# Kernel optimization log

Hardware: AMD Instinct MI355X
Metric: run time of the kernel (lower is better)

The kernel has to match this reference:

```python
import jax, jax.numpy as jnp
import numpy as np
from jax import lax

DN = ('NCHW', 'OIHW', 'NCHW')
BN_EPS = 1e-5
LRELU_SLOPE = 0.01


def conv_block(x, w1, b1, w2, b2, gamma, bn_bias):
    # Conv2d(512->256, k=1) -> Conv2d(256->512, k=3, pad=1) -> LeakyReLU -> BatchNorm2d(512)
    y = lax.conv_general_dilated(x, w1, (1, 1), 'VALID', dimension_numbers=DN)
    y = y + b1[None, :, None, None]
    y = lax.conv_general_dilated(y, w2, (1, 1), 'SAME', dimension_numbers=DN)
    y = y + b2[None, :, None, None]
    y = jnp.where(y > 0, y, LRELU_SLOPE * y)
    # BatchNorm2d in training mode: batch statistics over (B, H, W) per channel
    mean = jnp.mean(y, axis=(0, 2, 3))
    var = jnp.var(y, axis=(0, 2, 3))
    y = (y - mean[None, :, None, None]) * lax.rsqrt(var + BN_EPS)[None, :, None, None]
    return y * gamma[None, :, None, None] + bn_bias[None, :, None, None]


def setup_inputs() -> dict:
    key = jax.random.key(0)
    ks = jax.random.split(key, 9)
    B, C, H, W = 8, 512, 32, 32
    x = jax.random.normal(ks[0], (B, C, H, W), dtype=jnp.float32)
    x1 = jax.random.normal(ks[1], (B, C, H, W), dtype=jnp.float32)
    x2 = jax.random.normal(ks[2], (B, C, H, W), dtype=jnp.float32)
    w1 = jax.random.normal(ks[3], (256, 512, 1, 1), dtype=jnp.float32) * 0.02
    b1 = jnp.zeros((256,), dtype=jnp.float32)
    w2 = jax.random.normal(ks[4], (512, 256, 3, 3), dtype=jnp.float32) * 0.02
    b2 = jnp.zeros((512,), dtype=jnp.float32)
    gamma = jnp.ones((512,), dtype=jnp.float32)
    bn_bias = jnp.zeros((512,), dtype=jnp.float32)
    beta = jax.random.normal(ks[5], (1,), dtype=jnp.float32)  # Parameter(zeros(1)) in torch; random so output is non-trivial
    return {"x": x, "x1": x1, "x2": x2, "w1": w1, "b1": b1, "w2": w2,
            "b2": b2, "gamma": gamma, "bn_bias": bn_bias, "beta": beta}


def reference(x, x1, x2, w1, b1, w2, b2, gamma, bn_bias, beta):
    B, C, H, W = x1.shape
    N = H * W
    F1 = conv_block(x1, w1, b1, w2, b2, gamma, bn_bias).reshape(B, C, N)   # [B, C, N]
    F2 = conv_block(x2, w1, b1, w2, b2, gamma, bn_bias).reshape(B, C, N)   # [B, C, N]
    scores = jnp.einsum('bcn,bdn->bcd', F1, F2)                            # [B, C, C]
    attention = jax.nn.softmax(scores, axis=-1)
    out = jnp.einsum('bcd,bdn->bcn', attention, x.reshape(B, C, N))
    return beta * out.reshape(B, C, H, W)
```

## Files before the change

### kernel.cpp

```cpp
#include <hip/hip_runtime.h>


typedef __attribute__((ext_vector_type(8))) short bfrag;
typedef __attribute__((ext_vector_type(4))) float facc;

__device__ __forceinline__ unsigned short bf16_rn(float v) {
  unsigned u = __float_as_uint(v);
  return (unsigned short)((u + 0x7fffu + ((u >> 16) & 1u)) >> 16);
}

__device__ __forceinline__ void dma16(const void* g, const void* lds) {
  __builtin_amdgcn_global_load_lds(
      (const __attribute__((address_space(1))) unsigned int*)g,
      (__attribute__((address_space(3))) unsigned int*)(unsigned int)(unsigned long long)(const char*)lds,
      16, 0, 0);
}

__global__ __launch_bounds__(256) void prologue(
    const float* __restrict__ x1, const float* __restrict__ x2,
    const float* __restrict__ w2, unsigned char* __restrict__ x12timg,
    unsigned short* __restrict__ w2s, float* __restrict__ statsz) {
  int bid = blockIdx.x;
  int t = threadIdx.x;
  if (bid < 8192) {
    __shared__ float tile[32][33];
    int p0 = (bid & 31) * 32, ci0 = ((bid >> 5) & 15) * 32, z = bid >> 9;
    const float* src = (z < 8) ? x1 + (size_t)z * 524288 : x2 + (size_t)(z - 8) * 524288;
    {
      int ci_l = t >> 5, p_l = t & 31;
#pragma unroll
      for (int j = 0; j < 4; j++)
        tile[ci_l + 8 * j][p_l] = src[(size_t)(ci0 + ci_l + 8 * j) * 1024 + p0 + p_l];
    }
    __syncthreads();
    {
      int p_l = t >> 3, cg = (t & 7) * 4;
      unsigned short hh[4], ll[4];
#pragma unroll
      for (int j = 0; j < 4; j++) {
        float v = tile[cg + j][p_l];
        hh[j] = bf16_rn(v);
        ll[j] = bf16_rn(v - __uint_as_float((unsigned)hh[j] << 16));
      }
      int px = p0 + p_l, row = px & 127, panel = px >> 7;
      int c = ci0 + cg, kc = c >> 6, ck = (c >> 3) & 7;
      int slot = ck ^ (row & 7);
      size_t byte = (((size_t)(z * 8 + panel) * 8 + kc) * 128 + row) * 256 + slot * 16 + (c & 7) * 2;
      *(ushort4*)(x12timg + byte) = make_ushort4(hh[0], hh[1], hh[2], hh[3]);
      *(ushort4*)(x12timg + byte + 128) = make_ushort4(ll[0], ll[1], ll[2], ll[3]);
    }
  } else {
    int co = bid - 8192;
    if (co < 40) statsz[co * 256 + t] = 0.f;
    int panel = co >> 7, co_l = co & 127;
    int chunk = t >> 5, q = (t >> 3) & 3, e = t & 7;
    int slot = q ^ (co_l & 7);
    const float* src = w2 + ((size_t)co * 256 + t) * 9;
#pragma unroll
    for (int tap = 0; tap < 9; tap++) {
      float v = src[tap];
      unsigned short h = bf16_rn(v);
      unsigned short l = bf16_rn(v - __uint_as_float((unsigned)h << 16));
      int P = (panel * 8 + chunk) * 9 + tap;
      size_t us = (size_t)P * 8192 + co_l * 64 + slot * 8 + e;
      w2s[us] = h;
      w2s[us ^ 32] = l;
    }
  }
}

__global__ __launch_bounds__(256) void transpose_split_x(
    const float* __restrict__ x, unsigned char* __restrict__ img) {
  __shared__ float tile[32][33];
  int z = blockIdx.z;
  const float* src = x + (size_t)z * 524288;
  int ci0 = blockIdx.y * 32, p0 = blockIdx.x * 32;
  int t = threadIdx.x;
  {
    int ci_l = t >> 5, p_l = t & 31;
#pragma unroll
    for (int j = 0; j < 4; j++)
      tile[ci_l + 8 * j][p_l] = src[(size_t)(ci0 + ci_l + 8 * j) * 1024 + p0 + p_l];
  }
  __syncthreads();
  {
    int p_l = t >> 3, cg = (t & 7) * 4;
    unsigned short hh[4], ll[4];
#pragma unroll
    for (int j = 0; j < 4; j++) {
      float v = tile[cg + j][p_l];
      hh[j] = bf16_rn(v);
      ll[j] = bf16_rn(v - __uint_as_float((unsigned)hh[j] << 16));
    }
    int px = p0 + p_l, row = px & 127, panel = px >> 7;
    int c = ci0 + cg, kc = c >> 6, ck = (c >> 3) & 7;
    int slot = ck ^ (row & 7);
    size_t byte = (((size_t)(z * 8 + panel) * 8 + kc) * 128 + row) * 256 + slot * 16 + (c & 7) * 2;
    *(ushort4*)(img + byte) = make_ushort4(hh[0], hh[1], hh[2], hh[3]);
    *(ushort4*)(img + byte + 128) = make_ushort4(ll[0], ll[1], ll[2], ll[3]);
  }
}

template <int KTOT, int EPI, int AF32, int KSPLIT>
__global__ __launch_bounds__(256, 2) void gemm_nt(
    const void* __restrict__ Asrc, long long aZS, int aKC,
    const unsigned char* __restrict__ Bimg, long long bZS, int bKC,
    void* __restrict__ out0,
    const float* __restrict__ p0, const float* __restrict__ p1,
    const float* __restrict__ p2, const float* __restrict__ p3) {
  __shared__ __attribute__((aligned(16))) unsigned char smem[49152];
  int t = threadIdx.x;
  int z = blockIdx.z;
  int zb = z, kh = 0;
  if (KSPLIT) { zb = z & 7; kh = z >> 3; }
  int m0 = blockIdx.y * 128, n0 = blockIdx.x * 64;
  int w = t >> 6, lane = t & 63;
  int lm = lane & 15, q = lane >> 4;
  int mh = (w & 1) * 64, nh = (w >> 1) * 32;
  const unsigned char* Abase = (const unsigned char*)Asrc + (size_t)zb * aZS +
      (size_t)(m0 >> 7) * ((size_t)aKC << 15) + (size_t)w * 8192 + (size_t)lane * 16;
  const unsigned char* Bbase = Bimg + (size_t)zb * bZS +
      (size_t)(n0 >> 7) * ((size_t)bKC << 15) + (size_t)(n0 & 127) * 256 +
      (size_t)w * 4096 + (size_t)lane * 16;
  facc acc[4][2] = {};
  for (int k0 = 0; k0 < KTOT; k0 += 64) {
    int kc = (KSPLIT ? kh * (KTOT / 64) : 0) + (k0 >> 6);
    __syncthreads();
    if (AF32) {
      const float* Af = (const float*)Asrc;
#pragma unroll
      for (int j = 0; j < 8; j++) {
        int idx = t + 256 * j;
        int row = idx >> 4, c4 = idx & 15;
        float4 v = *(const float4*)(Af + (size_t)(m0 + row) * KTOT + k0 + c4 * 4);
        unsigned short h0 = bf16_rn(v.x), h1 = bf16_rn(v.y), h2 = bf16_rn(v.z), h3 = bf16_rn(v.w);
        unsigned short l0 = bf16_rn(v.x - __uint_as_float((unsigned)h0 << 16));
        unsigned short l1 = bf16_rn(v.y - __uint_as_float((unsigned)h1 << 16));
        unsigned short l2 = bf16_rn(v.z - __uint_as_float((unsigned)h2 << 16));
        unsigned short l3 = bf16_rn(v.w - __uint_as_float((unsigned)h3 << 16));
        int base = row * 256 + (((c4 >> 1) ^ (row & 7)) * 16) + (c4 & 1) * 8;
        *(ushort4*)(smem + base) = make_ushort4(h0, h1, h2, h3);
        *(ushort4*)(smem + base + 128) = make_ushort4(l0, l1, l2, l3);
      }
    } else {
      const unsigned char* ap = Abase + ((size_t)kc << 15);
#pragma unroll
      for (int j = 0; j < 8; j++) dma16(ap + j * 1024, smem + w * 8192 + j * 1024);
    }
    {
      const unsigned char* bp = Bbase + ((size_t)kc << 15);
#pragma unroll
      for (int j = 0; j < 4; j++) dma16(bp + j * 1024, smem + 32768 + w * 4096 + j * 1024);
    }
    __syncthreads();
#pragma unroll
    for (int ks = 0; ks < 2; ks++) {
      bfrag ah[4], al[4], bh[2], bl[2];
#pragma unroll
      for (int mt = 0; mt < 4; mt++) {
        int m = mh + mt * 16 + lm;
        int phys = ((ks * 4 + q) ^ (m & 7)) * 16;
        const unsigned char* p = smem + m * 256 + phys;
        ah[mt] = *(const bfrag*)p;
        al[mt] = *(const bfrag*)(p + 128);
      }
#pragma unroll
      for (int nt = 0; nt < 2; nt++) {
        int n = nh + nt * 16 + lm;
        int phys = ((ks * 4 + q) ^ (n & 7)) * 16;
        const unsigned char* p = smem + 32768 + n * 256 + phys;
        bh[nt] = *(const bfrag*)p;
        bl[nt] = *(const bfrag*)(p + 128);
      }
#pragma unroll
      for (int mt = 0; mt < 4; mt++)
#pragma unroll
        for (int nt = 0; nt < 2; nt++) {
          acc[mt][nt] = __builtin_amdgcn_mfma_f32_16x16x32_bf16(ah[mt], bh[nt], acc[mt][nt], 0, 0, 0);
          acc[mt][nt] = __builtin_amdgcn_mfma_f32_16x16x32_bf16(ah[mt], bl[nt], acc[mt][nt], 0, 0, 0);
          acc[mt][nt] = __builtin_amdgcn_mfma_f32_16x16x32_bf16(al[mt], bh[nt], acc[mt][nt], 0, 0, 0);
        }
    }
  }
  if (EPI == 0) {
    unsigned char* Yimg = (unsigned char*)out0;
    int g = zb;
#pragma unroll
    for (int mt = 0; mt < 4; mt++) {
      int mb = m0 + mh + mt * 16 + q * 4;
      int ch = mb >> 5, chunk = (mb >> 3) & 3, e2 = (mb & 7) * 2;
#pragma unroll
      for (int nt = 0; nt < 2; nt++) {
        int px = n0 + nh + nt * 16 + lm;
        int gy = px >> 5, gx = px & 31;
        int slot = chunk ^ ((gx + 1) & 7);
        size_t base = ((size_t)((g * 8 + ch) * 32 + gy)) * 4096 + gx * 128 + slot * 16 + e2;
        unsigned short hh[4], ll[4];
#pragma unroll
        for (int r = 0; r < 4; r++) {
          float v = acc[mt][nt][r] + p0[mb + r];
          hh[r] = bf16_rn(v);
          ll[r] = bf16_rn(v - __uint_as_float((unsigned)hh[r] << 16));
        }
        *(ushort4*)(Yimg + base) = make_ushort4(hh[0], hh[1], hh[2], hh[3]);
        *(ushort4*)(Yimg + (base ^ 64)) = make_ushort4(ll[0], ll[1], ll[2], ll[3]);
      }
    }
  } else if (EPI == 1) {
    float* S = (float*)out0 + (size_t)kh * 2097152;
    const float* stats = p0;
    const float* rowsum = p1;
    const float* gamma = p2;
    const float* bnb = p3;
    float a2v[2], t2v[2], r2v[2];
#pragma unroll
    for (int nt = 0; nt < 2; nt++) {
      int d = n0 + nh + nt * 16 + lm;
      float mu = stats[512 + d] * (1.f / 8192.f);
      float var = stats[1536 + d] * (1.f / 8192.f) - mu * mu;
      float a = gamma[d] * rsqrtf(var + 1e-5f);
      a2v[nt] = a;
      t2v[nt] = bnb[d] - mu * a;
      r2v[nt] = rowsum[(8 + zb) * 512 + d];
    }
#pragma unroll
    for (int mt = 0; mt < 4; mt++)
#pragma unroll
      for (int r = 0; r < 4; r++) {
        int cc = m0 + mh + mt * 16 + q * 4 + r;
        float mu = stats[cc] * (1.f / 8192.f);
        float var = stats[1024 + cc] * (1.f / 8192.f) - mu * mu;
        float a1 = gamma[cc] * rsqrtf(var + 1e-5f);
        float t1 = bnb[cc] - mu * a1;
        float r1 = rowsum[zb * 512 + cc];
#pragma unroll
        for (int nt = 0; nt < 2; nt++) {
          int d = n0 + nh + nt * 16 + lm;
          float sc = a1 * a2v[nt] * acc[mt][nt][r];
          if (kh == 0)
            sc += a1 * t2v[nt] * r1 + t1 * a2v[nt] * r2v[nt] + 1024.f * t1 * t2v[nt];
          S[((size_t)(zb * 512 + cc)) * 512 + d] = sc;
        }
      }
  } else {
    float* O = (float*)out0;
    float sc = p0[0];
#pragma unroll
    for (int mt = 0; mt < 4; mt++)
#pragma unroll
      for (int r = 0; r < 4; r++) {
        int cc = m0 + mh + mt * 16 + q * 4 + r;
#pragma unroll
        for (int nt = 0; nt < 2; nt++) {
          int n = n0 + nh + nt * 16 + lm;
          O[((size_t)(zb * 512 + cc)) * 1024 + n] = sc * acc[mt][nt][r];
        }
      }
  }
}

__global__ __launch_bounds__(256, 2) void conv3x3_mfma(
    const unsigned char* __restrict__ Yimg, const unsigned short* __restrict__ w2s,
    const float* __restrict__ b2, unsigned char* __restrict__ Fimg,
    float* __restrict__ stats, float* __restrict__ rowsum) {
  __shared__ __attribute__((aligned(16))) unsigned char smem[67584];
  const int WOFF = 34816;
  int t = threadIdx.x;
  int g = blockIdx.z;
  int panel = blockIdx.y;
  int co_base = panel * 128;
  int y0 = blockIdx.x * 4;
  int w = t >> 6, lane = t & 63;
  int lm = lane & 15, q = lane >> 4;
  int co_half = (w & 1) * 64, px_half = (w >> 1) * 64;
  int pha = (q ^ (lm & 7)) * 16;
  int px_l[4], row_l[4], x_l[4];
#pragma unroll
  for (int i = 0; i < 4; i++) {
    px_l[i] = px_half + i * 16 + lm;
    row_l[i] = px_l[i] >> 5;
    x_l[i] = px_l[i] & 31;
  }
  const unsigned char* w2sb = (const unsigned char*)w2s + (((size_t)panel * 72) << 14);
  auto stageW = [&](int P) {
    const unsigned char* srcp = w2sb + (((size_t)P) << 14) + (w * 4) * 1024 + lane * 16;
    unsigned char* dstp = smem + WOFF + ((P & 1) << 14) + (w * 4) * 1024;
#pragma unroll
    for (int j = 0; j < 4; j++) dma16(srcp + j * 1024, dstp + j * 1024);
  };
  auto stageStrip = [&](int slot, int gy, int cc) {
    unsigned char* dst = smem + slot * 4352 + 128 + w * 1024;
    if ((unsigned)gy < 32u) {
      const unsigned char* srcp = Yimg +
          ((size_t)((g * 8 + cc) * 32 + gy)) * 4096 + w * 1024 + lane * 16;
      dma16(srcp, dst);
    } else {
      *(uint4*)(dst + lane * 16) = make_uint4(0u, 0u, 0u, 0u);
    }
  };
  for (int u = t; u < 2176; u += 256)
    *(uint4*)(smem + (size_t)u * 16) = make_uint4(0u, 0u, 0u, 0u);
  __syncthreads();
  stageW(0);
  stageStrip(0, y0 - 1, 0);
  stageStrip(1, y0 + 0, 0);
  stageStrip(2, y0 + 1, 0);
  stageStrip(3, y0 + 2, 0);
  __syncthreads();
  facc acc[4][4] = {};
#pragma unroll 1
  for (int c = 0; c < 8; c++) {
    int base6 = (c * 6) & 7;
#pragma unroll
    for (int tap = 0; tap < 9; tap++) {
      const int dy = tap / 3, dx = tap % 3;
      int p = c * 9 + tap;
      if (p < 71) stageW(p + 1);
      if (tap == 0) {
        stageStrip((base6 + 4) & 7, y0 + 3, c);
        stageStrip((base6 + 5) & 7, y0 + 4, c);
        if (c < 7) {
          stageStrip((base6 + 6) & 7, y0 - 1, c + 1);
          stageStrip((base6 + 7) & 7, y0 + 0, c + 1);
        }
      } else if (tap == 3) {
        if (c < 7) stageStrip(base6, y0 + 1, c + 1);
      } else if (tap == 6) {
        if (c < 7) stageStrip((base6 + 1) & 7, y0 + 2, c + 1);
      }
      const unsigned char* wb = smem + WOFF + ((p & 1) << 14);
      bfrag ah[4], al[4], bh[4], bl[4];
#pragma unroll
      for (int j = 0; j < 4; j++) {
        int co_r = co_half + j * 16 + lm;
        const unsigned char* pa = wb + co_r * 128;
        ah[j] = *(const bfrag*)(pa + pha);
        al[j] = *(const bfrag*)(pa + (pha ^ 64));
      }
#pragma unroll
      for (int i = 0; i < 4; i++) {
        int xh = x_l[i] + dx;
        int slot = (base6 + row_l[i] + dy) & 7;
        const unsigned char* pb = smem + slot * 4352 + xh * 128;
        int ph = (q ^ (xh & 7)) * 16;
        bh[i] = *(const bfrag*)(pb + ph);
        bl[i] = *(const bfrag*)(pb + (ph ^ 64));
      }
#pragma unroll
      for (int j = 0; j < 4; j++)
#pragma unroll
        for (int i = 0; i < 4; i++) {
          acc[j][i] = __builtin_amdgcn_mfma_f32_16x16x32_bf16(ah[j], bh[i], acc[j][i], 0, 0, 0);
          acc[j][i] = __builtin_amdgcn_mfma_f32_16x16x32_bf16(ah[j], bl[i], acc[j][i], 0, 0, 0);
          acc[j][i] = __builtin_amdgcn_mfma_f32_16x16x32_bf16(al[j], bh[i], acc[j][i], 0, 0, 0);
        }
      __syncthreads();
    }
  }
  int grp = g >> 3;
  int px0 = blockIdx.x * 128;
#pragma unroll
  for (int j = 0; j < 4; j++) {
#pragma unroll
    for (int r = 0; r < 4; r++) {
      int co = co_base + co_half + j * 16 + q * 4 + r;
      int row = co & 127;
      float bb = b2[co];
      float s = 0.f, s2 = 0.f;
#pragma unroll
      for (int i = 0; i < 4; i++) {
        float v = acc[j][i][r] + bb;
        v = v > 0.f ? v : 0.01f * v;
        unsigned short h = bf16_rn(v);
        unsigned short l = bf16_rn(v - __uint_as_float((unsigned)h << 16));
        int px = px0 + px_l[i];
        int kc = px >> 6, ck = (px >> 3) & 7;
        int slot = ck ^ (row & 7);
        size_t byte = (((size_t)(g * 4 + panel) * 16 + kc) * 128 + row) * 256 +
                      slot * 16 + (px & 7) * 2;
        *(unsigned short*)(Fimg + byte) = h;
        *(unsigned short*)(Fimg + byte + 128) = l;
        s += v;
        s2 = fmaf(v, v, s2);
      }
#pragma unroll
      for (int d = 1; d <= 8; d <<= 1) {
        s += __shfl_xor(s, d);
        s2 += __shfl_xor(s2, d);
      }
      if (lm == 0) {
        atomicAdd(&stats[grp * 512 + co], s);
        atomicAdd(&stats[1024 + grp * 512 + co], s2);
        atomicAdd(&rowsum[g * 512 + co], s);
      }
    }
  }
}

__global__ __launch_bounds__(256) void softmax_rows(const float* __restrict__ S,
                                                    unsigned char* __restrict__ attimg) {
  int rowg = blockIdx.x;
  int z = rowg >> 9, c = rowg & 511;
  const float* p = S + (size_t)rowg * 512;
  const float* p1 = p + 2097152;
  int t = threadIdx.x;
  float2 va = *(const float2*)(p + 2 * t);
  float2 vb = *(const float2*)(p1 + 2 * t);
  float vx = va.x + vb.x, vy = va.y + vb.y;
  float mx = fmaxf(vx, vy);
#pragma unroll
  for (int d = 32; d >= 1; d >>= 1) mx = fmaxf(mx, __shfl_xor(mx, d));
  __shared__ float sred[8];
  int wave = t >> 6, lane = t & 63;
  if (lane == 0) sred[wave] = mx;
  __syncthreads();
  float m4 = fmaxf(fmaxf(sred[0], sred[1]), fmaxf(sred[2], sred[3]));
  float ex = expf(vx - m4), ey = expf(vy - m4);
  float s = ex + ey;
#pragma unroll
  for (int d = 32; d >= 1; d >>= 1) s += __shfl_xor(s, d);
  if (lane == 0) sred[4 + wave] = s;
  __syncthreads();
  float inv = 1.f / (sred[4] + sred[5] + sred[6] + sred[7]);
  float px_ = ex * inv, py_ = ey * inv;
  unsigned short h0 = bf16_rn(px_), h1 = bf16_rn(py_);
  unsigned short l0 = bf16_rn(px_ - __uint_as_float((unsigned)h0 << 16));
  unsigned short l1 = bf16_rn(py_ - __uint_as_float((unsigned)h1 << 16));
  int rowl = c & 127, panel = c >> 7;
  int d0 = 2 * t;
  int kc = d0 >> 6, ck = (d0 >> 3) & 7;
  int slot = ck ^ (rowl & 7);
  size_t byte = (((size_t)(z * 4 + panel) * 8 + kc) * 128 + rowl) * 256 +
                slot * 16 + (d0 & 7) * 2;
  *(ushort2*)(attimg + byte) = make_ushort2(h0, h1);
  *(ushort2*)(attimg + byte + 128) = make_ushort2(l0, l1);
}

extern "C" void kernel_launch(void* const* d_in, const int* in_sizes, int n_in,
                              void* d_out, int out_size, void* d_ws, size_t ws_size,
                              hipStream_t stream) {
  const float* x = (const float*)d_in[0];
  const float* x1 = (const float*)d_in[1];
  const float* x2 = (const float*)d_in[2];
  const float* w1 = (const float*)d_in[3];
  const float* b1 = (const float*)d_in[4];
  const float* w2 = (const float*)d_in[5];
  const float* b2 = (const float*)d_in[6];
  const float* gamma = (const float*)d_in[7];
  const float* bnb = (const float*)d_in[8];
  const float* beta = (const float*)d_in[9];
  float* out = (float*)d_out;
  unsigned char* wsb = (unsigned char*)d_ws;

  unsigned char* x12timg = wsb;
  unsigned char* Fimg = wsb;
  unsigned char* xtimg = wsb;
  unsigned char* attimg = wsb + 16777216;
  unsigned char* Yimg = wsb + 33554432;
  float* S = (float*)(wsb + 33554432);
  unsigned short* w2s = (unsigned short*)(wsb + 50331648);
  float* stats = (float*)(wsb + 55050240);
  float* rowsum = (float*)(wsb + 55058432);

  prologue<<<8704, 256, 0, stream>>>(x1, x2, w2, x12timg, w2s, stats);
  gemm_nt<512, 0, 1, 0><<<dim3(16, 2, 16), 256, 0, stream>>>(
      w1, 0LL, 0, x12timg, 2097152LL, 8, Yimg, b1, nullptr, nullptr, nullptr);
  conv3x3_mfma<<<dim3(8, 4, 16), 256, 0, stream>>>(
      Yimg, w2s, b2, Fimg, stats, rowsum);
  gemm_nt<512, 1, 0, 1><<<dim3(8, 4, 16), 256, 0, stream>>>(
      Fimg, 2097152LL, 16, Fimg + (size_t)8 * 2097152, 2097152LL, 16,
      S, stats, rowsum, gamma, bnb);
  transpose_split_x<<<dim3(32, 16, 8), 256, 0, stream>>>(x, xtimg);
  softmax_rows<<<4096, 256, 0, stream>>>(S, attimg);
  gemm_nt<512, 2, 0, 0><<<dim3(16, 4, 8), 256, 0, stream>>>(
      attimg, 1048576LL, 8, xtimg, 2097152LL, 8, out, beta, nullptr, nullptr, nullptr);
}
```

Measured before the change: 291.3 us.

## Double-buffer MFMA operand fragments in registers across conv3x3 taps

The 3x3 convolution main loop now loads the LDS fragments for the next tap into a second register set while the current tap's MFMAs run. This hides LDS read latency behind matrix math. To keep the next tap's data resident, weight staging moves to a distance of two: two weight tiles are prefetched up front and stageW(p+2) is issued each step. The cost is roughly twice the fragment registers, which could spill or limit occupancy under launch_bounds(256,2).

```diff
diff --git a/kernel.cpp b/kernel.cpp
--- a/kernel.cpp
+++ b/kernel.cpp
@@ -259,6 +259,27 @@
   }
 }
 
+#define READ_FRAGS(S, CN, TAPN)                                                 \
+  {                                                                             \
+    const int dyn_ = (TAPN) / 3, dxn_ = (TAPN) % 3;                             \
+    int b6n_ = ((CN) * 6) & 7;                                                  \
+    const unsigned char* wbn_ =                                                 \
+        smem + WOFF + (((((CN) * 9 + (TAPN)) & 1)) << 14);                      \
+    _Pragma("unroll") for (int j_ = 0; j_ < 4; j_++) {                          \
+      const unsigned char* pa_ = wbn_ + (co_half + j_ * 16 + lm) * 128;         \
+      fAh[S][j_] = *(const bfrag*)(pa_ + pha);                                  \
+      fAl[S][j_] = *(const bfrag*)(pa_ + (pha ^ 64));                           \
+    }                                                                           \
+    _Pragma("unroll") for (int i_ = 0; i_ < 4; i_++) {                          \
+      int xh_ = x_l[i_] + dxn_;                                                 \
+      int slot_ = (b6n_ + row_l[i_] + dyn_) & 7;                                \
+      const unsigned char* pb_ = smem + slot_ * 4352 + xh_ * 128;               \
+      int ph_ = (q ^ (xh_ & 7)) * 16;                                           \
+      fBh[S][i_] = *(const bfrag*)(pb_ + ph_);                                  \
+      fBl[S][i_] = *(const bfrag*)(pb_ + (ph_ ^ 64));                           \
+    }                                                                           \
+  }
+
 __global__ __launch_bounds__(256, 2) void conv3x3_mfma(
     const unsigned char* __restrict__ Yimg, const unsigned short* __restrict__ w2s,
     const float* __restrict__ b2, unsigned char* __restrict__ Fimg,
@@ -302,59 +323,55 @@
     *(uint4*)(smem + (size_t)u * 16) = make_uint4(0u, 0u, 0u, 0u);
   __syncthreads();
   stageW(0);
+  stageW(1);
   stageStrip(0, y0 - 1, 0);
   stageStrip(1, y0 + 0, 0);
   stageStrip(2, y0 + 1, 0);
   stageStrip(3, y0 + 2, 0);
   __syncthreads();
   facc acc[4][4] = {};
+  bfrag fAh[2][4], fAl[2][4], fBh[2][4], fBl[2][4];
+  READ_FRAGS(0, 0, 0)
 #pragma unroll 1
-  for (int c = 0; c < 8; c++) {
-    int base6 = (c * 6) & 7;
-#pragma unroll
-    for (int tap = 0; tap < 9; tap++) {
-      const int dy = tap / 3, dx = tap % 3;
-      int p = c * 9 + tap;
-      if (p < 71) stageW(p + 1);
-      if (tap == 0) {
-        stageStrip((base6 + 4) & 7, y0 + 3, c);
-        stageStrip((base6 + 5) & 7, y0 + 4, c);
-        if (c < 7) {
-          stageStrip((base6 + 6) & 7, y0 - 1, c + 1);
-          stageStrip((base6 + 7) & 7, y0 + 0, c + 1);
-        }
-      } else if (tap == 3) {
-        if (c < 7) stageStrip(base6, y0 + 1, c + 1);
-      } else if (tap == 6) {
-        if (c < 7) stageStrip((base6 + 1) & 7, y0 + 2, c + 1);
-      }
-      const unsigned char* wb = smem + WOFF + ((p & 1) << 14);
-      bfrag ah[4], al[4], bh[4], bl[4];
-#pragma unroll
-      for (int j = 0; j < 4; j++) {
-        int co_r = co_half + j * 16 + lm;
-        const unsigned char* pa = wb + co_r * 128;
-        ah[j] = *(const bfrag*)(pa + pha);
-        al[j] = *(const bfrag*)(pa + (pha ^ 64));
-      }
-#pragma unroll
-      for (int i = 0; i < 4; i++) {
-        int xh = x_l[i] + dx;
-        int slot = (base6 + row_l[i] + dy) & 7;
-        const unsigned char* pb = smem + slot * 4352 + xh * 128;
-        int ph = (q ^ (xh & 7)) * 16;
-        bh[i] = *(const bfrag*)(pb + ph);
-        bl[i] = *(const bfrag*)(pb + (ph ^ 64));
-      }
-#pragma unroll
-      for (int j = 0; j < 4; j++)
-#pragma unroll
-        for (int i = 0; i < 4; i++) {
-          acc[j][i] = __builtin_amdgcn_mfma_f32_16x16x32_bf16(ah[j], bh[i], acc[j][i], 0, 0, 0);
-          acc[j][i] = __builtin_amdgcn_mfma_f32_16x16x32_bf16(ah[j], bl[i], acc[j][i], 0, 0, 0);
-          acc[j][i] = __builtin_amdgcn_mfma_f32_16x16x32_bf16(al[j], bh[i], acc[j][i], 0, 0, 0);
-        }
-      __syncthreads();
+  for (int cc = 0; cc < 4; cc++) {
+#pragma unroll
+    for (int half = 0; half < 2; half++) {
+#pragma unroll
+      for (int tap = 0; tap < 9; tap++) {
+        const int parity = (half + tap) & 1;
+        int c = cc * 2 + half;
+        int p = c * 9 + tap;
+        if (p < 70) stageW(p + 2);
+        int base6 = (c * 6) & 7;
+        if (tap == 0) {
+          stageStrip((base6 + 4) & 7, y0 + 3, c);
+          stageStrip((base6 + 5) & 7, y0 + 4, c);
+          if (c < 7) {
+            stageStrip((base6 + 6) & 7, y0 - 1, c + 1);
+            stageStrip((base6 + 7) & 7, y0 + 0, c + 1);
+          }
+        } else if (tap == 3) {
+          if (c < 7) stageStrip(base6, y0 + 1, c + 1);
+        } else if (tap == 6) {
+          if (c < 7) stageStrip((base6 + 1) & 7, y0 + 2, c + 1);
+        }
+        if (p < 71) {
+          if (tap < 8) {
+            READ_FRAGS(parity ^ 1, c, tap + 1)
+          } else {
+            READ_FRAGS(parity ^ 1, c + 1, 0)
+          }
+        }
+#pragma unroll
+        for (int j = 0; j < 4; j++)
+#pragma unroll
+          for (int i = 0; i < 4; i++) {
+            acc[j][i] = __builtin_amdgcn_mfma_f32_16x16x32_bf16(fAh[parity][j], fBh[parity][i], acc[j][i], 0, 0, 0);
+            acc[j][i] = __builtin_amdgcn_mfma_f32_16x16x32_bf16(fAh[parity][j], fBl[parity][i], acc[j][i], 0, 0, 0);
+            acc[j][i] = __builtin_amdgcn_mfma_f32_16x16x32_bf16(fAl[parity][j], fBh[parity][i], acc[j][i], 0, 0, 0);
+          }
+        __syncthreads();
+      }
     }
   }
   int grp = g >> 3;
```

Result: faster. 284.8 us (-2.3%).

## Shrink conv3x3 tile and load weights directly from global in fragment layout

Applied to the files above, without the earlier changes.

The conv3x3 kernel tile drops from 128 output channels × 128 pixels to 128 × 64 (2 image rows), so each wave now owns 32 channels × 64 pixels. Weight fragments are no longer staged through LDS with async copies; the prologue writes w2 pre-arranged in per-lane MFMA fragment order, and each wave reads its fragments straight from global memory. LDS use falls from about 66 KB to about 26 KB and the launch bound rises to 4 blocks/CU, doubling the grid to gain occupancy. The cost is weight fragment loads on the critical path each tap, with no prefetch, plus a larger halo re-read fraction per block.

```diff
diff --git a/kernel.cpp b/kernel.cpp
--- a/kernel.cpp
+++ b/kernel.cpp
@@ -52,9 +52,9 @@
   } else {
     int co = bid - 8192;
     if (co < 40) statsz[co * 256 + t] = 0.f;
-    int panel = co >> 7, co_l = co & 127;
+    int panel = co >> 7, w = (co >> 5) & 3, j = (co >> 4) & 1, lm = co & 15;
     int chunk = t >> 5, q = (t >> 3) & 3, e = t & 7;
-    int slot = q ^ (co_l & 7);
+    int lane = q * 16 + lm;
     const float* src = w2 + ((size_t)co * 256 + t) * 9;
 #pragma unroll
     for (int tap = 0; tap < 9; tap++) {
@@ -62,9 +62,9 @@
       unsigned short h = bf16_rn(v);
       unsigned short l = bf16_rn(v - __uint_as_float((unsigned)h << 16));
       int P = (panel * 8 + chunk) * 9 + tap;
-      size_t us = (size_t)P * 8192 + co_l * 64 + slot * 8 + e;
+      size_t us = (size_t)P * 8192 + w * 2048 + j * 1024 + lane * 8 + e;
       w2s[us] = h;
-      w2s[us ^ 32] = l;
+      w2s[us + 512] = l;
     }
   }
 }
@@ -259,35 +259,20 @@
   }
 }
 
-__global__ __launch_bounds__(256, 2) void conv3x3_mfma(
+__global__ __launch_bounds__(256, 4) void conv3x3_mfma(
     const unsigned char* __restrict__ Yimg, const unsigned short* __restrict__ w2s,
     const float* __restrict__ b2, unsigned char* __restrict__ Fimg,
     float* __restrict__ stats, float* __restrict__ rowsum) {
-  __shared__ __attribute__((aligned(16))) unsigned char smem[67584];
-  const int WOFF = 34816;
+  __shared__ __attribute__((aligned(16))) unsigned char smem[26112];
   int t = threadIdx.x;
   int g = blockIdx.z;
   int panel = blockIdx.y;
   int co_base = panel * 128;
-  int y0 = blockIdx.x * 4;
+  int y0 = blockIdx.x * 2;
   int w = t >> 6, lane = t & 63;
   int lm = lane & 15, q = lane >> 4;
-  int co_half = (w & 1) * 64, px_half = (w >> 1) * 64;
-  int pha = (q ^ (lm & 7)) * 16;
-  int px_l[4], row_l[4], x_l[4];
-#pragma unroll
-  for (int i = 0; i < 4; i++) {
-    px_l[i] = px_half + i * 16 + lm;
-    row_l[i] = px_l[i] >> 5;
-    x_l[i] = px_l[i] & 31;
-  }
-  const unsigned char* w2sb = (const unsigned char*)w2s + (((size_t)panel * 72) << 14);
-  auto stageW = [&](int P) {
-    const unsigned char* srcp = w2sb + (((size_t)P) << 14) + (w * 4) * 1024 + lane * 16;
-    unsigned char* dstp = smem + WOFF + ((P & 1) << 14) + (w * 4) * 1024;
-#pragma unroll
-    for (int j = 0; j < 4; j++) dma16(srcp + j * 1024, dstp + j * 1024);
-  };
+  const unsigned char* w2sb = (const unsigned char*)w2s +
+      (((size_t)panel * 72) << 14) + (size_t)w * 4096 + (size_t)lane * 16;
   auto stageStrip = [&](int slot, int gy, int cc) {
     unsigned char* dst = smem + slot * 4352 + 128 + w * 1024;
     if ((unsigned)gy < 32u) {
@@ -298,72 +283,71 @@
       *(uint4*)(dst + lane * 16) = make_uint4(0u, 0u, 0u, 0u);
     }
   };
-  for (int u = t; u < 2176; u += 256)
+  for (int u = t; u < 1632; u += 256)
     *(uint4*)(smem + (size_t)u * 16) = make_uint4(0u, 0u, 0u, 0u);
   __syncthreads();
-  stageW(0);
   stageStrip(0, y0 - 1, 0);
   stageStrip(1, y0 + 0, 0);
   stageStrip(2, y0 + 1, 0);
   stageStrip(3, y0 + 2, 0);
   __syncthreads();
-  facc acc[4][4] = {};
+  facc acc[2][4] = {};
 #pragma unroll 1
   for (int c = 0; c < 8; c++) {
-    int base6 = (c * 6) & 7;
-#pragma unroll
+    int base4 = (c * 4) % 6;
+#pragma unroll 1
     for (int tap = 0; tap < 9; tap++) {
-      const int dy = tap / 3, dx = tap % 3;
-      int p = c * 9 + tap;
-      if (p < 71) stageW(p + 1);
-      if (tap == 0) {
-        stageStrip((base6 + 4) & 7, y0 + 3, c);
-        stageStrip((base6 + 5) & 7, y0 + 4, c);
-        if (c < 7) {
-          stageStrip((base6 + 6) & 7, y0 - 1, c + 1);
-          stageStrip((base6 + 7) & 7, y0 + 0, c + 1);
-        }
-      } else if (tap == 3) {
-        if (c < 7) stageStrip(base6, y0 + 1, c + 1);
-      } else if (tap == 6) {
-        if (c < 7) stageStrip((base6 + 1) & 7, y0 + 2, c + 1);
-      }
-      const unsigned char* wb = smem + WOFF + ((p & 1) << 14);
-      bfrag ah[4], al[4], bh[4], bl[4];
-#pragma unroll
-      for (int j = 0; j < 4; j++) {
-        int co_r = co_half + j * 16 + lm;
-        const unsigned char* pa = wb + co_r * 128;
-        ah[j] = *(const bfrag*)(pa + pha);
-        al[j] = *(const bfrag*)(pa + (pha ^ 64));
-      }
+      int dy = tap / 3, dx = tap - dy * 3;
+      const unsigned char* wp = w2sb + (((size_t)(c * 9 + tap)) << 14);
+      bfrag wh[2], wl[2];
+#pragma unroll
+      for (int j = 0; j < 2; j++) {
+        wh[j] = *(const bfrag*)(wp + j * 2048);
+        wl[j] = *(const bfrag*)(wp + j * 2048 + 1024);
+      }
+      if (c < 7) {
+        if (tap == 0) {
+          int p4 = base4 + 4; p4 = p4 < 6 ? p4 : p4 - 6;
+          int p5 = base4 + 5; p5 = p5 < 6 ? p5 : p5 - 6;
+          stageStrip(p4, y0 - 1, c + 1);
+          stageStrip(p5, y0 + 0, c + 1);
+        } else if (tap == 3) {
+          stageStrip(base4, y0 + 1, c + 1);
+        } else if (tap == 6) {
+          stageStrip(base4 + 1, y0 + 2, c + 1);
+        }
+      }
+      int bd = base4 + dy;
+      int r0 = bd < 6 ? bd : bd - 6;
+      int r1 = bd + 1 < 6 ? bd + 1 : bd - 5;
+      bfrag bh[4], bl[4];
 #pragma unroll
       for (int i = 0; i < 4; i++) {
-        int xh = x_l[i] + dx;
-        int slot = (base6 + row_l[i] + dy) & 7;
+        int xh = (i & 1) * 16 + lm + dx;
+        int slot = (i >> 1) ? r1 : r0;
         const unsigned char* pb = smem + slot * 4352 + xh * 128;
         int ph = (q ^ (xh & 7)) * 16;
         bh[i] = *(const bfrag*)(pb + ph);
         bl[i] = *(const bfrag*)(pb + (ph ^ 64));
       }
 #pragma unroll
-      for (int j = 0; j < 4; j++)
+      for (int j = 0; j < 2; j++)
 #pragma unroll
         for (int i = 0; i < 4; i++) {
-          acc[j][i] = __builtin_amdgcn_mfma_f32_16x16x32_bf16(ah[j], bh[i], acc[j][i], 0, 0, 0);
-          acc[j][i] = __builtin_amdgcn_mfma_f32_16x16x32_bf16(ah[j], bl[i], acc[j][i], 0, 0, 0);
-          acc[j][i] = __builtin_amdgcn_mfma_f32_16x16x32_bf16(al[j], bh[i], acc[j][i], 0, 0, 0);
+          acc[j][i] = __builtin_amdgcn_mfma_f32_16x16x32_bf16(wh[j], bh[i], acc[j][i], 0, 0, 0);
+          acc[j][i] = __builtin_amdgcn_mfma_f32_16x16x32_bf16(wh[j], bl[i], acc[j][i], 0, 0, 0);
+          acc[j][i] = __builtin_amdgcn_mfma_f32_16x16x32_bf16(wl[j], bh[i], acc[j][i], 0, 0, 0);
         }
       __syncthreads();
     }
   }
   int grp = g >> 3;
-  int px0 = blockIdx.x * 128;
-#pragma unroll
-  for (int j = 0; j < 4; j++) {
+  int px0 = blockIdx.x * 64;
+#pragma unroll
+  for (int j = 0; j < 2; j++) {
 #pragma unroll
     for (int r = 0; r < 4; r++) {
-      int co = co_base + co_half + j * 16 + q * 4 + r;
+      int co = co_base + w * 32 + j * 16 + q * 4 + r;
       int row = co & 127;
       float bb = b2[co];
       float s = 0.f, s2 = 0.f;
@@ -373,7 +357,7 @@
         v = v > 0.f ? v : 0.01f * v;
         unsigned short h = bf16_rn(v);
         unsigned short l = bf16_rn(v - __uint_as_float((unsigned)h << 16));
-        int px = px0 + px_l[i];
+        int px = px0 + i * 16 + lm;
         int kc = px >> 6, ck = (px >> 3) & 7;
         int slot = ck ^ (row & 7);
         size_t byte = (((size_t)(g * 4 + panel) * 16 + kc) * 128 + row) * 256 +
@@ -465,7 +449,7 @@
   prologue<<<8704, 256, 0, stream>>>(x1, x2, w2, x12timg, w2s, stats);
   gemm_nt<512, 0, 1, 0><<<dim3(16, 2, 16), 256, 0, stream>>>(
       w1, 0LL, 0, x12timg, 2097152LL, 8, Yimg, b1, nullptr, nullptr, nullptr);
-  conv3x3_mfma<<<dim3(8, 4, 16), 256, 0, stream>>>(
+  conv3x3_mfma<<<dim3(16, 4, 16), 256, 0, stream>>>(
       Yimg, w2s, b2, Fimg, stats, rowsum);
   gemm_nt<512, 1, 0, 1><<<dim3(8, 4, 16), 256, 0, stream>>>(
       Fimg, 2097152LL, 16, Fimg + (size_t)8 * 2097152, 2097152LL, 16,
```

Result: no change. 291.8 us (+0.2%).
